# Performance work log

Hardware: AMD Instinct MI355X
Metric: run time of the kernel (lower is better)

The kernel has to match this reference:

```python
import jax, jax.numpy as jnp
import numpy as np

# Constants matching module_cfg
H, W = 256, 256          # cfg.img_size
N_GAUSS, CF = 1024, 15   # number of Gaussians, appearance feature channels (feat_dim-1)


def setup_inputs() -> dict:
    key = jax.random.key(0)
    k0, k1, k2, k3, k4 = jax.random.split(key, 5)
    # Gaussians in front of an identity camera (z in [2,4])
    xy = jax.random.normal(k0, (N_GAUSS, 2), dtype=jnp.float32) * 0.5
    z = jax.random.uniform(k1, (N_GAUSS, 1), minval=2.0, maxval=4.0, dtype=jnp.float32)
    xyzs = jnp.concatenate([xy, z], axis=-1)[None]                      # [1,N,3]
    feats = jax.random.uniform(k2, (1, N_GAUSS, CF), dtype=jnp.float32)  # [1,N,15]
    opac = jax.random.uniform(k3, (1, N_GAUSS, 1), minval=0.3, maxval=0.9, dtype=jnp.float32)
    # PSD 3D covariances (small splats)
    A = jax.random.normal(k4, (N_GAUSS, 3, 3), dtype=jnp.float32) * 0.02
    cov = (jnp.einsum('nij,nkj->nik', A, A) + 1e-4 * jnp.eye(3, dtype=jnp.float32))[None]  # [1,N,3,3]
    fx = fy = 500.0
    K = jnp.array([[[fx, 0.0, W / 2.0], [0.0, fy, H / 2.0], [0.0, 0.0, 1.0]]], dtype=jnp.float32)
    E = jnp.eye(4, dtype=jnp.float32)[None]  # world-to-camera
    return {"xyzs_observation": xyzs, "appearance_feats": feats, "opacity": opac,
            "cov": cov, "K": K, "E": E}


def _render(xyzs, feats, opac, cov, K, E):
    """Fused 3DGS rasterization: geometry/sort computed once, all channels composited in one pass
    (the original loops the full pipeline per 3-channel slice)."""
    fx, fy = K[0, 0, 0], K[0, 1, 1]
    px, py = K[0, 0, 2], K[0, 1, 2]
    R = E[0, :3, :3]
    tr = E[0, :3, 3]
    p = xyzs[0]                      # [N,3] world
    t = p @ R.T + tr                 # [N,3] camera space
    tz = t[:, 2]
    # EWA Jacobian with frustum clamping (as in 3DGS computeCov2D)
    limx = 1.3 * (W / (2.0 * fx))    # 1.3 * tanfovx
    limy = 1.3 * (H / (2.0 * fy))
    txc = jnp.clip(t[:, 0] / tz, -limx, limx) * tz
    tyc = jnp.clip(t[:, 1] / tz, -limy, limy) * tz
    z2 = tz * tz
    zeros = jnp.zeros_like(tz)
    J = jnp.stack([jnp.stack([fx / tz, zeros, -fx * txc / z2], -1),
                   jnp.stack([zeros, fy / tz, -fy * tyc / z2], -1)], -2)  # [N,2,3]
    Tm = J @ R                                                           # [N,2,3]
    c2 = jnp.einsum('nij,njk,nlk->nil', Tm, cov[0], Tm)                  # [N,2,2]
    a = c2[:, 0, 0] + 0.3  # low-pass dilation as in 3DGS
    b = c2[:, 0, 1]
    c = c2[:, 1, 1] + 0.3
    det = a * c - b * b
    inv = 1.0 / det
    cA, cB, cC = c * inv, -b * inv, a * inv                              # conic
    # projected pixel-space means (NDC->pixel as in 3DGS: fx*x/z + px - 0.5)
    ux = fx * t[:, 0] / tz + px - 0.5
    uy = fy * t[:, 1] / tz + py - 0.5
    valid = (tz > 0.2) & (det > 0.0)  # frustum / degenerate cull
    # feat = [appearance, ones] -> last channel renders accumulated alpha
    feat = jnp.concatenate([feats[0], jnp.ones_like(opac[0])], axis=-1)  # [N,C]
    op = jnp.where(valid, opac[0, :, 0], 0.0)
    # global front-to-back depth sort
    order = jnp.argsort(tz)
    ux, uy, cA, cB, cC, op = (v[order] for v in (ux, uy, cA, cB, cC, op))
    feat = feat[order]
    # pixel grid (integer pixel coords, as in the CUDA kernel)
    yg, xg = jnp.meshgrid(jnp.arange(H, dtype=jnp.float32),
                          jnp.arange(W, dtype=jnp.float32), indexing='ij')
    xg = xg.reshape(-1)  # [P]
    yg = yg.reshape(-1)
    dx = ux[None, :] - xg[:, None]   # [P,N]
    dy = uy[None, :] - yg[:, None]
    power = -0.5 * (cA[None, :] * dx * dx + cC[None, :] * dy * dy) - cB[None, :] * dx * dy
    g = jnp.where(power <= 0.0, jnp.exp(jnp.minimum(power, 0.0)), 0.0)
    alpha = jnp.minimum(0.99, op[None, :] * g)
    alpha = jnp.where(alpha < 1.0 / 255.0, 0.0, alpha)  # per-splat cull as in kernel
    trans = jnp.cumprod(1.0 - alpha, axis=1)
    Tprev = jnp.concatenate([jnp.ones((alpha.shape[0], 1), alpha.dtype), trans[:, :-1]], axis=1)
    wgt = Tprev * alpha              # [P,N] compositing weights
    img = wgt @ feat                 # [P,C]  all channels in one pass (bg = 0)
    img = img.reshape(H, W, -1)[None]  # [1,H,W,C]
    return img[..., :-1], img[..., -1]


def reference(xyzs_observation, appearance_feats, opacity, cov, K, E):
    return _render(xyzs_observation, appearance_feats, opacity, cov, K, E)
```

## Files before the change

### kernel.cpp

```cpp
#include <hip/hip_runtime.h>
#include <math.h>

#define HH 256
#define WW 256
#define NG 1024
#define CF 15

struct G {
    float ux, uy, hA, hB, hC, op, pthr, bx, by;
    unsigned kz;
};

__device__ __forceinline__ G geom(int i,
                                  const float* __restrict__ xyz,
                                  const float* __restrict__ opac,
                                  const float* __restrict__ cov,
                                  const float* __restrict__ s )
{
    const float fx = s[0], fy = s[1], px = s[2], py = s[3];
    const float R00 = s[4],  R01 = s[5],  R02 = s[6];
    const float R10 = s[7],  R11 = s[8],  R12 = s[9];
    const float R20 = s[10], R21 = s[11], R22 = s[12];
    const float tr0 = s[13], tr1 = s[14], tr2 = s[15];

    const float p0 = xyz[i * 3 + 0], p1 = xyz[i * 3 + 1], p2 = xyz[i * 3 + 2];
    const float t0 = R00 * p0 + R01 * p1 + R02 * p2 + tr0;
    const float t1 = R10 * p0 + R11 * p1 + R12 * p2 + tr1;
    const float tz = R20 * p0 + R21 * p1 + R22 * p2 + tr2;

    const float limx = 1.3f * ((float)WW / (2.0f * fx));
    const float limy = 1.3f * ((float)HH / (2.0f * fy));
    const float itz = 1.0f / tz;
    const float txz = t0 * itz, tyz = t1 * itz;
    const float txc = fminf(fmaxf(txz, -limx), limx) * tz;
    const float tyc = fminf(fmaxf(tyz, -limy), limy) * tz;
    const float z2 = tz * tz;
    const float J00 = fx * itz, J02 = -fx * txc / z2;
    const float J11 = fy * itz, J12 = -fy * tyc / z2;

    const float T00 = J00 * R00 + J02 * R20;
    const float T01 = J00 * R01 + J02 * R21;
    const float T02 = J00 * R02 + J02 * R22;
    const float T10 = J11 * R10 + J12 * R20;
    const float T11 = J11 * R11 + J12 * R21;
    const float T12 = J11 * R12 + J12 * R22;

    const float* C = cov + i * 9;
    const float M00 = T00 * C[0] + T01 * C[3] + T02 * C[6];
    const float M01 = T00 * C[1] + T01 * C[4] + T02 * C[7];
    const float M02 = T00 * C[2] + T01 * C[5] + T02 * C[8];
    const float M10 = T10 * C[0] + T11 * C[3] + T12 * C[6];
    const float M11 = T10 * C[1] + T11 * C[4] + T12 * C[7];
    const float M12 = T10 * C[2] + T11 * C[5] + T12 * C[8];

    const float A2 = M00 * T00 + M01 * T01 + M02 * T02 + 0.3f;
    const float B2 = M00 * T10 + M01 * T11 + M02 * T12;
    const float C2 = M10 * T10 + M11 * T11 + M12 * T12 + 0.3f;

    const float det = A2 * C2 - B2 * B2;
    const float inv = 1.0f / det;
    const float cA = C2 * inv, cB = -B2 * inv, cC = A2 * inv;

    G r;
    r.ux = fx * txz + px - 0.5f;
    r.uy = fy * tyz + py - 0.5f;
    r.hA = -0.5f * cA;
    r.hB = -cB;
    r.hC = -0.5f * cC;

    const bool valid = (tz > 0.2f) && (det > 0.0f);
    r.op = valid ? opac[i] : 0.0f;
    r.pthr = (r.op > 0.0f) ? logf(1.0f / (255.0f * r.op)) : 3.0e38f;

    if (r.op > 0.0f) {
        const float L = -2.0f * r.pthr;
        r.bx = sqrtf(L * A2);
        r.by = sqrtf(L * C2);
    } else {
        r.bx = -1.0e30f;
        r.by = -1.0e30f;
    }

    unsigned u = __float_as_uint(tz);
    r.kz = (u & 0x80000000u) ? ~u : (u | 0x80000000u);
    return r;
}

__global__ __launch_bounds__(256)
void render_fused(const float* __restrict__ xyz,
                  const float* __restrict__ feats,
                  const float* __restrict__ opac,
                  const float* __restrict__ cov,
                  const float* __restrict__ Kp,
                  const float* __restrict__ Ep,
                  float* __restrict__ out0,
                  float* __restrict__ out1)
{
    __shared__ float sKE[16];
    __shared__ unsigned long long skey[NG];
    __shared__ float4 sA[256];
    __shared__ float4 sB[256];
    __shared__ float4 sF[256][4];
    __shared__ int wcnt[4];

    const int tid = threadIdx.x;

    if (tid == 0) {
        sKE[0]  = Kp[0]; sKE[1]  = Kp[4]; sKE[2]  = Kp[2]; sKE[3]  = Kp[5];
        sKE[4]  = Ep[0]; sKE[5]  = Ep[1]; sKE[6]  = Ep[2];
        sKE[7]  = Ep[4]; sKE[8]  = Ep[5]; sKE[9]  = Ep[6];
        sKE[10] = Ep[8]; sKE[11] = Ep[9]; sKE[12] = Ep[10];
        sKE[13] = Ep[3]; sKE[14] = Ep[7]; sKE[15] = Ep[11];
    }
    __syncthreads();

    const int tx = blockIdx.x & 15, ty = blockIdx.x >> 4;
    const int x0 = tx * 16, y0 = ty * 16;
    const float xf = (float)(x0 + (tid & 15));
    const float yf = (float)(y0 + (tid >> 4));
    const float tlx = (float)x0, thx = (float)(x0 + 15);
    const float tly = (float)y0, thy = (float)(y0 + 15);

    int tot = 0;
    for (int c = 0; c < NG / 256; ++c) {
        const int g = c * 256 + tid;
        const G gg = geom(g, xyz, opac, cov, sKE);
        const bool hit = (gg.ux + gg.bx >= tlx) && (gg.ux - gg.bx <= thx) &&
                         (gg.uy + gg.by >= tly) && (gg.uy - gg.by <= thy);

        const unsigned long long bal = __ballot(hit);
        const int lane = tid & 63, w = tid >> 6;
        if (lane == 0) wcnt[w] = __popcll(bal);
        __syncthreads();
        int base = tot;
#pragma unroll
        for (int q = 0; q < 4; ++q) base += (q < w) ? wcnt[q] : 0;
        if (hit) {
            const int slot = base + __popcll(bal & ((1ull << lane) - 1ull));
            skey[slot] = ((unsigned long long)gg.kz << 32) | (unsigned)g;
        }
        tot += wcnt[0] + wcnt[1] + wcnt[2] + wcnt[3];
        __syncthreads();
    }

    float T = 1.0f;
    float acc[16];
#pragma unroll
    for (int c = 0; c < 16; ++c) acc[c] = 0.0f;

    if (tot > 0) {
        int K = 1;
        while (K < tot) K <<= 1;
        for (int e = tot + tid; e < K; e += 256) skey[e] = ~0ull;
        __syncthreads();

        for (int k = 2; k <= K; k <<= 1) {
            for (int j = k >> 1; j > 0; j >>= 1) {
                for (int e = tid; e < K; e += 256) {
                    const int ixj = e ^ j;
                    if (ixj > e) {
                        const unsigned long long a = skey[e];
                        const unsigned long long b = skey[ixj];
                        const bool up = ((e & k) == 0);
                        if (up ? (a > b) : (a < b)) {
                            skey[e] = b;
                            skey[ixj] = a;
                        }
                    }
                }
                __syncthreads();
            }
        }

        const int nrun = (tot + 255) >> 8;
        for (int run = 0; run < nrun; ++run) {
            const int rbase = run << 8;
            const int s = rbase + tid;
            if (s < tot) {
                const int idx = (int)(unsigned)(skey[s] & 0xffffffffull);
                const G gg = geom(idx, xyz, opac, cov, sKE);
                sA[tid] = make_float4(gg.ux, gg.uy, gg.hA, gg.hB);
                sB[tid] = make_float4(gg.hC, gg.op, gg.pthr, 0.0f);
                const float* f = feats + idx * CF;
                sF[tid][0] = make_float4(f[0],  f[1],  f[2],  f[3]);
                sF[tid][1] = make_float4(f[4],  f[5],  f[6],  f[7]);
                sF[tid][2] = make_float4(f[8],  f[9],  f[10], f[11]);
                sF[tid][3] = make_float4(f[12], f[13], f[14], 1.0f);
            }
            __syncthreads();

            const int cnt = min(256, tot - rbase);
            for (int e = 0; e < cnt; ++e) {
                const float4 a = sA[e];
                const float4 b = sB[e];
                const float dx = a.x - xf;
                const float dy = a.y - yf;
                float power = a.z * dx * dx;
                power = fmaf(a.w, dx * dy, power);
                power = fmaf(b.x, dy * dy, power);
                if (power <= 0.0f && power >= b.z) {
                    const float alpha = fminf(0.99f, b.y * __expf(power));
                    const float wgt = T * alpha;
                    const float4 f0 = sF[e][0];
                    const float4 f1 = sF[e][1];
                    const float4 f2 = sF[e][2];
                    const float4 f3 = sF[e][3];
                    acc[0]  = fmaf(wgt, f0.x, acc[0]);
                    acc[1]  = fmaf(wgt, f0.y, acc[1]);
                    acc[2]  = fmaf(wgt, f0.z, acc[2]);
                    acc[3]  = fmaf(wgt, f0.w, acc[3]);
                    acc[4]  = fmaf(wgt, f1.x, acc[4]);
                    acc[5]  = fmaf(wgt, f1.y, acc[5]);
                    acc[6]  = fmaf(wgt, f1.z, acc[6]);
                    acc[7]  = fmaf(wgt, f1.w, acc[7]);
                    acc[8]  = fmaf(wgt, f2.x, acc[8]);
                    acc[9]  = fmaf(wgt, f2.y, acc[9]);
                    acc[10] = fmaf(wgt, f2.z, acc[10]);
                    acc[11] = fmaf(wgt, f2.w, acc[11]);
                    acc[12] = fmaf(wgt, f3.x, acc[12]);
                    acc[13] = fmaf(wgt, f3.y, acc[13]);
                    acc[14] = fmaf(wgt, f3.z, acc[14]);
                    acc[15] = fmaf(wgt, f3.w, acc[15]);
                    T *= (1.0f - alpha);
                }
                if ((e & 31) == 31 && __all(T < 1e-4f)) break;
            }
            if (__syncthreads_and(T < 1e-4f)) break;
        }
    }

    const int pix = (y0 + (tid >> 4)) * WW + (x0 + (tid & 15));
#pragma unroll
    for (int c = 0; c < CF; ++c) out0[pix * CF + c] = acc[c];
    out1[pix] = acc[15];
}

extern "C" void kernel_launch(void* const* d_in, const int* in_sizes, int n_in,
                              void* d_out, int out_size, void* d_ws, size_t ws_size,
                              hipStream_t stream) {
    const float* xyz   = (const float*)d_in[0];
    const float* feats = (const float*)d_in[1];
    const float* opac  = (const float*)d_in[2];
    const float* cov   = (const float*)d_in[3];
    const float* Kp    = (const float*)d_in[4];
    const float* Ep    = (const float*)d_in[5];

    float* out0 = (float*)d_out;
    float* out1 = out0 + HH * WW * CF;

    render_fused<<<256, 256, 0, stream>>>(xyz, feats, opac, cov, Kp, Ep,
                                          out0, out1);
}
```

Measured before the change: 89.14 us.

## Split geometry into precompute kernel and use wave-shuffle sort for small lists

Per-Gaussian projection and conic math now runs once in a separate kernel and is written to workspace, together with padded float4 features. Before, each of the 256 tile blocks recomputed it for all 1024 Gaussians and again for the splats it kept. The culling pass is restructured to issue all four chunk ballots before a single barrier instead of two barriers per chunk. Tiles with at most 64 hits are sorted with a register bitonic sort using wave shuffles instead of the shared-memory network. This adds a second launch and global-memory round trips for the precomputed data.

```diff
diff --git a/kernel.cpp b/kernel.cpp
--- a/kernel.cpp
+++ b/kernel.cpp
@@ -6,22 +6,25 @@
 #define NG 1024
 #define CF 15
 
-struct G {
-    float ux, uy, hA, hB, hC, op, pthr, bx, by;
-    unsigned kz;
-};
-
-__device__ __forceinline__ G geom(int i,
-                                  const float* __restrict__ xyz,
-                                  const float* __restrict__ opac,
-                                  const float* __restrict__ cov,
-                                  const float* __restrict__ s )
+__global__ __launch_bounds__(128)
+void geom_kernel(const float* __restrict__ xyz,
+                 const float* __restrict__ feats,
+                 const float* __restrict__ opac,
+                 const float* __restrict__ cov,
+                 const float* __restrict__ Kp,
+                 const float* __restrict__ Ep,
+                 float4* __restrict__ cullv,
+                 float4* __restrict__ gA,
+                 float4* __restrict__ gB,
+                 float4* __restrict__ feat4,
+                 unsigned* __restrict__ kz)
 {
-    const float fx = s[0], fy = s[1], px = s[2], py = s[3];
-    const float R00 = s[4],  R01 = s[5],  R02 = s[6];
-    const float R10 = s[7],  R11 = s[8],  R12 = s[9];
-    const float R20 = s[10], R21 = s[11], R22 = s[12];
-    const float tr0 = s[13], tr1 = s[14], tr2 = s[15];
+    const int i = blockIdx.x * 128 + threadIdx.x;
+
+    const float fx = Kp[0], px = Kp[2], fy = Kp[4], py = Kp[5];
+    const float R00 = Ep[0], R01 = Ep[1], R02 = Ep[2],  tr0 = Ep[3];
+    const float R10 = Ep[4], R11 = Ep[5], R12 = Ep[6],  tr1 = Ep[7];
+    const float R20 = Ep[8], R21 = Ep[9], R22 = Ep[10], tr2 = Ep[11];
 
     const float p0 = xyz[i * 3 + 0], p1 = xyz[i * 3 + 1], p2 = xyz[i * 3 + 2];
     const float t0 = R00 * p0 + R01 * p1 + R02 * p2 + tr0;
@@ -61,58 +64,52 @@
     const float inv = 1.0f / det;
     const float cA = C2 * inv, cB = -B2 * inv, cC = A2 * inv;
 
-    G r;
-    r.ux = fx * txz + px - 0.5f;
-    r.uy = fy * tyz + py - 0.5f;
-    r.hA = -0.5f * cA;
-    r.hB = -cB;
-    r.hC = -0.5f * cC;
+    const float ux = fx * txz + px - 0.5f;
+    const float uy = fy * tyz + py - 0.5f;
 
     const bool valid = (tz > 0.2f) && (det > 0.0f);
-    r.op = valid ? opac[i] : 0.0f;
-    r.pthr = (r.op > 0.0f) ? logf(1.0f / (255.0f * r.op)) : 3.0e38f;
-
-    if (r.op > 0.0f) {
-        const float L = -2.0f * r.pthr;
-        r.bx = sqrtf(L * A2);
-        r.by = sqrtf(L * C2);
-    } else {
-        r.bx = -1.0e30f;
-        r.by = -1.0e30f;
+    const float op = valid ? opac[i] : 0.0f;
+    const float pthr = (op > 0.0f) ? logf(1.0f / (255.0f * op)) : 3.0e38f;
+
+    float bx = -1.0e30f, by = -1.0e30f;
+    if (op > 0.0f) {
+        const float L = -2.0f * pthr;
+        bx = sqrtf(L * A2);
+        by = sqrtf(L * C2);
     }
 
     unsigned u = __float_as_uint(tz);
-    r.kz = (u & 0x80000000u) ? ~u : (u | 0x80000000u);
-    return r;
+    u = (u & 0x80000000u) ? ~u : (u | 0x80000000u);
+
+    cullv[i] = make_float4(ux, uy, bx, by);
+    gA[i]    = make_float4(ux, uy, -0.5f * cA, -cB);
+    gB[i]    = make_float4(-0.5f * cC, op, pthr, 0.0f);
+    kz[i]    = u;
+
+    const float* f = feats + i * CF;
+    feat4[i * 4 + 0] = make_float4(f[0],  f[1],  f[2],  f[3]);
+    feat4[i * 4 + 1] = make_float4(f[4],  f[5],  f[6],  f[7]);
+    feat4[i * 4 + 2] = make_float4(f[8],  f[9],  f[10], f[11]);
+    feat4[i * 4 + 3] = make_float4(f[12], f[13], f[14], 1.0f);
 }
 
 __global__ __launch_bounds__(256)
-void render_fused(const float* __restrict__ xyz,
-                  const float* __restrict__ feats,
-                  const float* __restrict__ opac,
-                  const float* __restrict__ cov,
-                  const float* __restrict__ Kp,
-                  const float* __restrict__ Ep,
-                  float* __restrict__ out0,
-                  float* __restrict__ out1)
+void render_kernel(const float4* __restrict__ cullv,
+                   const float4* __restrict__ gA,
+                   const float4* __restrict__ gB,
+                   const float4* __restrict__ feat4,
+                   const unsigned* __restrict__ kz,
+                   float* __restrict__ out0,
+                   float* __restrict__ out1)
 {
-    __shared__ float sKE[16];
     __shared__ unsigned long long skey[NG];
     __shared__ float4 sA[256];
     __shared__ float4 sB[256];
     __shared__ float4 sF[256][4];
-    __shared__ int wcnt[4];
+    __shared__ int wcnt16[16];
 
     const int tid = threadIdx.x;
-
-    if (tid == 0) {
-        sKE[0]  = Kp[0]; sKE[1]  = Kp[4]; sKE[2]  = Kp[2]; sKE[3]  = Kp[5];
-        sKE[4]  = Ep[0]; sKE[5]  = Ep[1]; sKE[6]  = Ep[2];
-        sKE[7]  = Ep[4]; sKE[8]  = Ep[5]; sKE[9]  = Ep[6];
-        sKE[10] = Ep[8]; sKE[11] = Ep[9]; sKE[12] = Ep[10];
-        sKE[13] = Ep[3]; sKE[14] = Ep[7]; sKE[15] = Ep[11];
-    }
-    __syncthreads();
+    const int lane = tid & 63, w = tid >> 6;
 
     const int tx = blockIdx.x & 15, ty = blockIdx.x >> 4;
     const int x0 = tx * 16, y0 = ty * 16;
@@ -121,27 +118,42 @@
     const float tlx = (float)x0, thx = (float)(x0 + 15);
     const float tly = (float)y0, thy = (float)(y0 + 15);
 
+    unsigned long long bal[4];
+    unsigned k32v[4];
+    bool hitv[4];
+#pragma unroll
+    for (int c = 0; c < 4; ++c) {
+        const int g = c * 256 + tid;
+        const float4 cu = cullv[g];
+        k32v[c] = kz[g];
+        hitv[c] = (cu.x + cu.z >= tlx) && (cu.x - cu.z <= thx) &&
+                  (cu.y + cu.w >= tly) && (cu.y - cu.w <= thy);
+        bal[c] = __ballot(hitv[c]);
+        if (lane == 0) wcnt16[c * 4 + w] = __popcll(bal[c]);
+    }
+    __syncthreads();
+
     int tot = 0;
-    for (int c = 0; c < NG / 256; ++c) {
-        const int g = c * 256 + tid;
-        const G gg = geom(g, xyz, opac, cov, sKE);
-        const bool hit = (gg.ux + gg.bx >= tlx) && (gg.ux - gg.bx <= thx) &&
-                         (gg.uy + gg.by >= tly) && (gg.uy - gg.by <= thy);
-
-        const unsigned long long bal = __ballot(hit);
-        const int lane = tid & 63, w = tid >> 6;
-        if (lane == 0) wcnt[w] = __popcll(bal);
-        __syncthreads();
-        int base = tot;
-#pragma unroll
-        for (int q = 0; q < 4; ++q) base += (q < w) ? wcnt[q] : 0;
-        if (hit) {
-            const int slot = base + __popcll(bal & ((1ull << lane) - 1ull));
-            skey[slot] = ((unsigned long long)gg.kz << 32) | (unsigned)g;
-        }
-        tot += wcnt[0] + wcnt[1] + wcnt[2] + wcnt[3];
-        __syncthreads();
-    }
+    int base_c[4];
+#pragma unroll
+    for (int c = 0; c < 4; ++c) {
+        int b = tot;
+#pragma unroll
+        for (int q = 0; q < 4; ++q) {
+            const int v = wcnt16[c * 4 + q];
+            if (q < w) b += v;
+            tot += v;
+        }
+        base_c[c] = b;
+    }
+#pragma unroll
+    for (int c = 0; c < 4; ++c) {
+        if (hitv[c]) {
+            const int slot = base_c[c] + __popcll(bal[c] & ((1ull << lane) - 1ull));
+            skey[slot] = ((unsigned long long)k32v[c] << 32) | (unsigned)(c * 256 + tid);
+        }
+    }
+    __syncthreads();
 
     float T = 1.0f;
     float acc[16];
@@ -149,26 +161,41 @@
     for (int c = 0; c < 16; ++c) acc[c] = 0.0f;
 
     if (tot > 0) {
-        int K = 1;
-        while (K < tot) K <<= 1;
-        for (int e = tot + tid; e < K; e += 256) skey[e] = ~0ull;
-        __syncthreads();
-
-        for (int k = 2; k <= K; k <<= 1) {
-            for (int j = k >> 1; j > 0; j >>= 1) {
-                for (int e = tid; e < K; e += 256) {
-                    const int ixj = e ^ j;
-                    if (ixj > e) {
-                        const unsigned long long a = skey[e];
-                        const unsigned long long b = skey[ixj];
-                        const bool up = ((e & k) == 0);
-                        if (up ? (a > b) : (a < b)) {
-                            skey[e] = b;
-                            skey[ixj] = a;
+        if (tot <= 64) {
+            unsigned long long key = (lane < tot) ? skey[lane] : ~0ull;
+            __syncthreads();
+#pragma unroll
+            for (int k = 2; k <= 64; k <<= 1) {
+                for (int j = k >> 1; j > 0; j >>= 1) {
+                    const unsigned long long part = __shfl_xor(key, j);
+                    const bool takeMin = (((lane & k) == 0) == ((lane & j) == 0));
+                    const bool partSmaller = (part < key);
+                    key = (takeMin == partSmaller) ? part : key;
+                }
+            }
+            if (w == 0) skey[lane] = key;
+            __syncthreads();
+        } else {
+            int K = 1;
+            while (K < tot) K <<= 1;
+            for (int e = tot + tid; e < K; e += 256) skey[e] = ~0ull;
+            __syncthreads();
+            for (int k = 2; k <= K; k <<= 1) {
+                for (int j = k >> 1; j > 0; j >>= 1) {
+                    for (int e = tid; e < K; e += 256) {
+                        const int ixj = e ^ j;
+                        if (ixj > e) {
+                            const unsigned long long a = skey[e];
+                            const unsigned long long b = skey[ixj];
+                            const bool up = ((e & k) == 0);
+                            if (up ? (a > b) : (a < b)) {
+                                skey[e] = b;
+                                skey[ixj] = a;
+                            }
                         }
                     }
+                    __syncthreads();
                 }
-                __syncthreads();
             }
         }
 
@@ -178,14 +205,12 @@
             const int s = rbase + tid;
             if (s < tot) {
                 const int idx = (int)(unsigned)(skey[s] & 0xffffffffull);
-                const G gg = geom(idx, xyz, opac, cov, sKE);
-                sA[tid] = make_float4(gg.ux, gg.uy, gg.hA, gg.hB);
-                sB[tid] = make_float4(gg.hC, gg.op, gg.pthr, 0.0f);
-                const float* f = feats + idx * CF;
-                sF[tid][0] = make_float4(f[0],  f[1],  f[2],  f[3]);
-                sF[tid][1] = make_float4(f[4],  f[5],  f[6],  f[7]);
-                sF[tid][2] = make_float4(f[8],  f[9],  f[10], f[11]);
-                sF[tid][3] = make_float4(f[12], f[13], f[14], 1.0f);
+                sA[tid] = gA[idx];
+                sB[tid] = gB[idx];
+                sF[tid][0] = feat4[(idx << 2) + 0];
+                sF[tid][1] = feat4[(idx << 2) + 1];
+                sF[tid][2] = feat4[(idx << 2) + 2];
+                sF[tid][3] = feat4[(idx << 2) + 3];
             }
             __syncthreads();
 
@@ -245,9 +270,18 @@
     const float* Kp    = (const float*)d_in[4];
     const float* Ep    = (const float*)d_in[5];
 
+    float* ws = (float*)d_ws;
+    float4*   cullv = (float4*)ws;
+    float4*   gAp   = (float4*)(ws + NG * 4);
+    float4*   gBp   = (float4*)(ws + NG * 8);
+    float4*   f4    = (float4*)(ws + NG * 12);
+    unsigned* kzp   = (unsigned*)(ws + NG * 28);
+
+    geom_kernel<<<8, 128, 0, stream>>>(xyz, feats, opac, cov, Kp, Ep,
+                                       cullv, gAp, gBp, f4, kzp);
+
     float* out0 = (float*)d_out;
     float* out1 = out0 + HH * WW * CF;
-
-    render_fused<<<256, 256, 0, stream>>>(xyz, feats, opac, cov, Kp, Ep,
-                                          out0, out1);
+    render_kernel<<<256, 256, 0, stream>>>(cullv, gAp, gBp, f4, kzp,
+                                           out0, out1);
 }
```

New measurement: 87.92 us. About the same (-1.4%).
